# Optimization experiments

Measured on AMD Instinct MI355X. Metric: run time of the kernel, lower is better.

Reference implementation:

```python
import jax, jax.numpy as jnp
import numpy as np

B = 48            # graph pairs
NQ, NC = 20, 16   # query / corpus node counts (corpus padded to NMAX)
NMAX = 20         # max_node_set_size
DN, DE = 16, 8    # raw node / edge feature dims
D = 32            # node_state_dim
EH = 64           # edge_hidden_sizes[-1]
EQ, EC = 80, 60   # edges per query / corpus graph
PROP = 5          # n_prop_layers
TEMP = 0.01       # sinkhorn temperature
ITERS = 20        # sinkhorn iterations
LAMBDA = 1.0
NTOT = B * (NQ + NC)
NE = B * (EQ + EC)
SRC, DST = np.triu_indices(NMAX, 1)   # nC2 = 190 node pairs
_indq = np.ones(NMAX, np.int32)
_indc = np.array([1] * NC + [0] * (NMAX - NC), np.int32)
NXOR = jnp.asarray((_indq[:, None] ^ _indc[None, :]).astype(np.float32))  # [20,20]


def _mlp2(x, w1, b1, w2, b2):
    return jnp.maximum(x @ w1 + b1, 0.0) @ w2 + b2


def _sinkhorn(log_alpha):
    la = log_alpha / TEMP
    for _ in range(ITERS):
        la = la - jax.nn.logsumexp(la, axis=2, keepdims=True)
        la = la - jax.nn.logsumexp(la, axis=1, keepdims=True)
    return jnp.exp(la)


def _edge_emb(H, adj, w1, b1, w2, b2):
    s, d = H[:, SRC], H[:, DST]            # [B,nC2,D] gathers
    e = adj[:, SRC, DST][..., None]        # [B,nC2,1]
    f = _mlp2(jnp.concatenate([s, d, e], -1), w1, b1, w2, b2)
    bk = _mlp2(jnp.concatenate([d, s, e], -1), w1, b1, w2, b2)
    return f + bk                          # bidirectional msg, [B,nC2,EH]


def _forward(node_features, edge_features, query_adj, corpus_adj,
             enc_nw, enc_nb, enc_ew, enc_eb,
             msg_w1, msg_b1, msg_w2, msg_b2,
             upd_w1, upd_b1, upd_w2, upd_b2,
             sink_w1, sink_b1, sink_w2, sink_b2,
             lrl_w1, lrl_b1, lrl_w2, lrl_b2,
             from_idx, to_idx):
    h = node_features @ enc_nw + enc_nb    # GMN encoder (linear MLPs)
    e = edge_features @ enc_ew + enc_eb
    for _ in range(PROP):                  # shared-param propagation
        msg = _mlp2(jnp.concatenate([h[from_idx], h[to_idx], e], -1),
                    msg_w1, msg_b1, msg_w2, msg_b2)
        agg = jax.ops.segment_sum(msg, to_idx, num_segments=NTOT)
        h = h + _mlp2(jnp.concatenate([agg, h], -1), upd_w1, upd_b1, upd_w2, upd_b2)
    hp = h.reshape(B, NQ + NC, D)          # split_and_stack (static sizes)
    Hq = hp[:, :NQ]
    Hc = jnp.pad(hp[:, NQ:], ((0, 0), (0, NMAX - NC), (0, 0)))
    tq = _mlp2(Hq, sink_w1, sink_b1, sink_w2, sink_b2)
    tc = _mlp2(Hc, sink_w1, sink_b1, sink_w2, sink_b2)
    cost = jnp.abs(tq[:, :, None, :] - tc[:, None, :, :]).sum(-1)  # cdist p=1
    P = _sinkhorn(-cost)                   # node transport plan [B,20,20]
    Eq = _edge_emb(Hq, query_adj, lrl_w1, lrl_b1, lrl_w2, lrl_b2)
    Ec = _edge_emb(Hc, corpus_adj, lrl_w1, lrl_b1, lrl_w2, lrl_b2)
    Pa, Pb = P[:, SRC, :], P[:, DST, :]
    straight = Pa[:, :, SRC] * Pb[:, :, DST]    # plan[src_i,src_j]*plan[dst_i,dst_j]
    cross = Pa[:, :, DST] * Pb[:, :, SRC]
    eT = straight + cross                  # use_max=False, no second sinkhorn
    aq = query_adj[:, SRC, DST].astype(jnp.int32)
    ac = corpus_adj[:, SRC, DST].astype(jnp.int32)
    pxor = (aq[:, :, None] ^ ac[:, None, :]).astype(P.dtype)
    ediff = Eq[:, :, None, :] - Ec[:, None, :, :]   # [B,nC2,nC2,EH]
    ecost = jnp.maximum(ediff, 0.0).sum(-1) + jnp.maximum(-ediff, 0.0).sum(-1)
    edge_align = (pxor * eT * ecost).sum((-1, -2))
    ndiff = Hq[:, :, None, :] - Hc[:, None, :, :]   # [B,20,20,D]
    ncost = jnp.maximum(ndiff, 0.0).sum(-1) + jnp.maximum(-ndiff, 0.0).sum(-1)
    node_align = (NXOR * P * ncost).sum((-1, -2))
    return edge_align + LAMBDA * node_align         # [B]


def setup_inputs():
    key = jax.random.key(0)
    rng = np.random.default_rng(0)
    base = (np.arange(B) * (NQ + NC))[:, None]
    fq = base + rng.integers(0, NQ, (B, EQ)); tq = base + rng.integers(0, NQ, (B, EQ))
    fc = base + NQ + rng.integers(0, NC, (B, EC)); tc = base + NQ + rng.integers(0, NC, (B, EC))
    from_idx = jnp.asarray(np.concatenate([fq, fc], 1).reshape(-1), jnp.int32)
    to_idx = jnp.asarray(np.concatenate([tq, tc], 1).reshape(-1), jnp.int32)
    qadj = rng.integers(0, 2, (B, NMAX, NMAX)).astype(np.float32)
    cadj = rng.integers(0, 2, (B, NMAX, NMAX)).astype(np.float32)
    cadj[:, NC:, :] = 0.0; cadj[:, :, NC:] = 0.0   # padded corpus nodes have no edges
    ks = iter(jax.random.split(key, 32))
    def w(shape, s=0.1):
        return jax.random.normal(next(ks), shape, jnp.float32) * s
    return {
        'node_features': w((NTOT, DN), 1.0),
        'edge_features': w((NE, DE), 1.0),
        'query_adj': jnp.asarray(qadj),
        'corpus_adj': jnp.asarray(cadj),
        'enc_nw': w((DN, D)), 'enc_nb': w((D,)),
        'enc_ew': w((DE, 16)), 'enc_eb': w((16,)),
        'msg_w1': w((2 * D + 16, EH)), 'msg_b1': w((EH,)),
        'msg_w2': w((EH, EH)), 'msg_b2': w((EH,)),
        'upd_w1': w((EH + D, EH)), 'upd_b1': w((EH,)),
        'upd_w2': w((EH, D)), 'upd_b2': w((D,)),
        'sink_w1': w((D, NMAX)), 'sink_b1': w((NMAX,)),
        'sink_w2': w((NMAX, NMAX)), 'sink_b2': w((NMAX,)),
        'lrl_w1': w((2 * D + 1, EH)), 'lrl_b1': w((EH,)),
        'lrl_w2': w((EH, EH)), 'lrl_b2': w((EH,)),
        'from_idx': from_idx, 'to_idx': to_idx,
        'graph_sizes': jnp.asarray(np.tile([NQ, NC], B), jnp.int32),
    }


def reference(node_features, edge_features, query_adj, corpus_adj,
              enc_nw, enc_nb, enc_ew, enc_eb,
              msg_w1, msg_b1, msg_w2, msg_b2,
              upd_w1, upd_b1, upd_w2, upd_b2,
              sink_w1, sink_b1, sink_w2, sink_b2,
              lrl_w1, lrl_b1, lrl_w2, lrl_b2,
              from_idx, to_idx, graph_sizes):
    return _forward(node_features, edge_features, query_adj, corpus_adj,
                    enc_nw, enc_nb, enc_ew, enc_eb,
                    msg_w1, msg_b1, msg_w2, msg_b2,
                    upd_w1, upd_b1, upd_w2, upd_b2,
                    sink_w1, sink_b1, sink_w2, sink_b2,
                    lrl_w1, lrl_b1, lrl_w2, lrl_b2,
                    from_idx, to_idx)
```

## Files before the change

### kernel.cpp

```cpp
#include <hip/hip_runtime.h>


constexpr int kB    = 48;
constexpr int kNM   = 20;
constexpr int kD    = 32;
constexpr int kNP   = 190;
constexpr int kNTOT = 1728;
constexpr int kIters = 20;
constexpr float kInvT = 100.0f;

__device__ __forceinline__ void pair_sd(int p, int& s, int& d) {
    int row = 0, rem = p;
    #pragma unroll
    for (int r = 0; r < 19; ++r) {
        int len = 19 - r;
        if (rem < len) { row = r; break; }
        rem -= len;
    }
    s = row; d = row + 1 + rem;
}

__device__ __forceinline__ float bc(float v, int k) {
    return __int_as_float(__builtin_amdgcn_readlane(__float_as_int(v), k));
}

__device__ __forceinline__ void lse20(float (&r)[20]) {
    float m01 = fmaxf(r[0], r[1]),  m23 = fmaxf(r[2], r[3]),
          m45 = fmaxf(r[4], r[5]),  m67 = fmaxf(r[6], r[7]),
          m89 = fmaxf(r[8], r[9]),  mab = fmaxf(r[10], r[11]),
          mcd = fmaxf(r[12], r[13]), mef = fmaxf(r[14], r[15]),
          mgh = fmaxf(r[16], r[17]), mij = fmaxf(r[18], r[19]);
    float n0 = fmaxf(m01, m23), n1 = fmaxf(m45, m67), n2 = fmaxf(m89, mab),
          n3 = fmaxf(mcd, mef), n4 = fmaxf(mgh, mij);
    float m = fmaxf(fmaxf(fmaxf(n0, n1), fmaxf(n2, n3)), n4);
    float e[20];
    #pragma unroll
    for (int k = 0; k < 20; ++k) e[k] = __expf(r[k] - m);
    float s01 = e[0] + e[1],  s23 = e[2] + e[3],  s45 = e[4] + e[5],
          s67 = e[6] + e[7],  s89 = e[8] + e[9],  sab = e[10] + e[11],
          scd = e[12] + e[13], sef = e[14] + e[15], sgh = e[16] + e[17],
          sij = e[18] + e[19];
    float t0 = s01 + s23, t1 = s45 + s67, t2 = s89 + sab,
          t3 = scd + sef, t4 = sgh + sij;
    float s = ((t0 + t1) + (t2 + t3)) + t4;
    float l = m + __logf(s);
    #pragma unroll
    for (int k = 0; k < 20; ++k) r[k] -= l;
}

__global__ void k_enc(const float* __restrict__ nf, const float* __restrict__ nw,
                      const float* __restrict__ nb, const float* __restrict__ ef,
                      const float* __restrict__ ew, const float* __restrict__ eb,
                      float* __restrict__ h, float* __restrict__ ee,
                      float* __restrict__ agg, float* __restrict__ out) {
    int tid = blockIdx.x * 256 + threadIdx.x;
    int stride = gridDim.x * 256;
    for (int i = tid; i < kNTOT * 32; i += stride) {
        int n = i >> 5, c = i & 31;
        float acc = nb[c];
        const float* row = nf + n * 16;
        #pragma unroll
        for (int k = 0; k < 16; ++k) acc = fmaf(row[k], nw[k * 32 + c], acc);
        h[i] = acc;
    }
    for (int i = tid; i < 6720 * 16; i += stride) {
        int n = i >> 4, c = i & 15;
        float acc = eb[c];
        const float* row = ef + n * 8;
        #pragma unroll
        for (int k = 0; k < 8; ++k) acc = fmaf(row[k], ew[k * 16 + c], acc);
        ee[i] = acc;
    }
    for (int i = tid; i < kNTOT * 64; i += stride) agg[i] = 0.f;
    if (tid < kB) out[tid] = 0.f;
}

__global__ void __launch_bounds__(256)
k_msg(const float* __restrict__ h, const float* __restrict__ ee,
      const int* __restrict__ fidx, const int* __restrict__ tidx,
      const float* __restrict__ w1, const float* __restrict__ b1,
      const float* __restrict__ w2, const float* __restrict__ b2,
      float* __restrict__ agg) {
    int w = threadIdx.x >> 6, lane = threadIdx.x & 63;
    int e0 = (blockIdx.x * 4 + w) * 2;
    int toj[2]; float xa[2], xb[2], acc[2], o[2];
    #pragma unroll
    for (int j = 0; j < 2; ++j) {
        int e = e0 + j;
        int fr = fidx[e]; toj[j] = tidx[e];
        xa[j] = h[(lane < 32 ? fr : toj[j]) * kD + (lane & 31)];
        xb[j] = ee[e * 16 + (lane & 15)];
        acc[j] = b1[lane];
    }
    #pragma unroll
    for (int k = 0; k < 64; ++k) {
        float w1k = w1[k * 64 + lane];
        #pragma unroll
        for (int j = 0; j < 2; ++j) acc[j] = fmaf(bc(xa[j], k), w1k, acc[j]);
    }
    #pragma unroll
    for (int k = 0; k < 16; ++k) {
        float w1k = w1[(64 + k) * 64 + lane];
        #pragma unroll
        for (int j = 0; j < 2; ++j) acc[j] = fmaf(bc(xb[j], k), w1k, acc[j]);
    }
    #pragma unroll
    for (int j = 0; j < 2; ++j) { acc[j] = fmaxf(acc[j], 0.f); o[j] = b2[lane]; }
    #pragma unroll
    for (int k = 0; k < 64; ++k) {
        float w2k = w2[k * 64 + lane];
        #pragma unroll
        for (int j = 0; j < 2; ++j) o[j] = fmaf(bc(acc[j], k), w2k, o[j]);
    }
    #pragma unroll
    for (int j = 0; j < 2; ++j) atomicAdd(&agg[toj[j] * 64 + lane], o[j]);
}

__global__ void __launch_bounds__(256)
k_upd(float* __restrict__ h, float* __restrict__ agg,
      const float* __restrict__ w1, const float* __restrict__ b1,
      const float* __restrict__ w2, const float* __restrict__ b2) {
    int w = threadIdx.x >> 6, lane = threadIdx.x & 63;
    int n0 = (blockIdx.x * 4 + w) * 2;
    float xa[2], xb[2], acc[2], o[2];
    #pragma unroll
    for (int j = 0; j < 2; ++j) {
        int n = n0 + j;
        xa[j] = agg[n * 64 + lane];
        agg[n * 64 + lane] = 0.f;
        xb[j] = h[n * kD + (lane & 31)];
        acc[j] = b1[lane];
    }
    #pragma unroll
    for (int k = 0; k < 64; ++k) {
        float w1k = w1[k * 64 + lane];
        #pragma unroll
        for (int j = 0; j < 2; ++j) acc[j] = fmaf(bc(xa[j], k), w1k, acc[j]);
    }
    #pragma unroll
    for (int k = 0; k < 32; ++k) {
        float w1k = w1[(64 + k) * 64 + lane];
        #pragma unroll
        for (int j = 0; j < 2; ++j) acc[j] = fmaf(bc(xb[j], k), w1k, acc[j]);
    }
    #pragma unroll
    for (int j = 0; j < 2; ++j) { acc[j] = fmaxf(acc[j], 0.f); o[j] = b2[lane & 31]; }
    #pragma unroll
    for (int k = 0; k < 64; ++k) {
        float w2k = w2[k * 32 + (lane & 31)];
        #pragma unroll
        for (int j = 0; j < 2; ++j) o[j] = fmaf(bc(acc[j], k), w2k, o[j]);
    }
    if (lane < 32) {
        #pragma unroll
        for (int j = 0; j < 2; ++j) h[(n0 + j) * kD + lane] += o[j];
    }
}

__global__ void k_sink_t(const float* __restrict__ h,
                         const float* __restrict__ w1, const float* __restrict__ b1,
                         const float* __restrict__ w2, const float* __restrict__ b2,
                         float* __restrict__ Hq, float* __restrict__ Hc,
                         float* __restrict__ tq, float* __restrict__ tc) {
    __shared__ float xs[4][32];
    __shared__ float hs[4][20];
    int w = threadIdx.x >> 6, lane = threadIdx.x & 63;
    int xcd = blockIdx.x & 7, slot = blockIdx.x >> 3;
    int b = xcd + 8 * (slot / 10);
    int task = (slot % 10) * 4 + w;
    int side = task >= 20;
    int i = task - side * 20;
    if (lane < 32) {
        float v;
        if (side == 0) v = h[(b * 36 + i) * kD + lane];
        else           v = (i < 16) ? h[(b * 36 + 20 + i) * kD + lane] : 0.f;
        (side ? Hc : Hq)[(b * kNM + i) * kD + lane] = v;
        xs[w][lane] = v;
    }
    __syncthreads();
    if (lane < kNM) {
        float acc = b1[lane];
        #pragma unroll
        for (int k = 0; k < kD; ++k) acc += xs[w][k] * w1[k * kNM + lane];
        hs[w][lane] = fmaxf(acc, 0.f);
    }
    __syncthreads();
    if (lane < kNM) {
        float o = b2[lane];
        #pragma unroll
        for (int k = 0; k < kNM; ++k) o += hs[w][k] * w2[k * kNM + lane];
        (side ? tc : tq)[(b * kNM + i) * kNM + lane] = o;
    }
}

__global__ void k_sinkhorn(const float* __restrict__ tq, const float* __restrict__ tc,
                           const float* __restrict__ Hq,
                           float* __restrict__ P, float* __restrict__ out) {
    __shared__ float tcS[400];
    __shared__ float tr[20 * 21];
    int b = blockIdx.x, lane = threadIdx.x;
    for (int i = lane; i < 400; i += 64) tcS[i] = tc[b * 400 + i];
    int i20 = lane < 20 ? lane : 0;
    float tqr[20];
    #pragma unroll
    for (int k = 0; k < 20; ++k) tqr[k] = tq[(b * 20 + i20) * 20 + k];
    __syncthreads();
    float r[20];
    #pragma unroll
    for (int j = 0; j < 20; ++j) {
        float c = 0.f;
        #pragma unroll
        for (int k = 0; k < 20; ++k) c += fabsf(tqr[k] - tcS[j * 20 + k]);
        r[j] = -c * kInvT;
    }
    for (int it = 0; it < kIters; ++it) {
        lse20(r);
        if (lane < 20) {
            #pragma unroll
            for (int j = 0; j < 20; ++j) tr[lane * 21 + j] = r[j];
        }
        __syncthreads();
        if (lane < 20) {
            #pragma unroll
            for (int i = 0; i < 20; ++i) r[i] = tr[i * 21 + lane];
        }
        __syncthreads();
        lse20(r);
        if (lane < 20) {
            #pragma unroll
            for (int i = 0; i < 20; ++i) tr[i * 21 + lane] = r[i];
        }
        __syncthreads();
        if (lane < 20) {
            #pragma unroll
            for (int j = 0; j < 20; ++j) r[j] = tr[lane * 21 + j];
        }
        __syncthreads();
    }
    float part = 0.f;
    if (lane < 20) {
        float pv[20];
        #pragma unroll
        for (int j = 0; j < 20; ++j) pv[j] = __expf(r[j]);
        float* Pb = P + b * 400 + lane * 20;
        #pragma unroll
        for (int j = 0; j < 20; ++j) Pb[j] = pv[j];
        float pr4 = (pv[16] + pv[17]) + (pv[18] + pv[19]);
        float l1 = 0.f;
        const float* hq = Hq + (b * 20 + lane) * 32;
        #pragma unroll
        for (int k = 0; k < 32; ++k) l1 += fabsf(hq[k]);
        part = pr4 * l1;
    }
    #pragma unroll
    for (int off = 32; off; off >>= 1) part += __shfl_down(part, off, 64);
    if (lane == 0) atomicAdd(&out[b], part);
}

__global__ void __launch_bounds__(256)
k_edge_emb(const float* __restrict__ Hq, const float* __restrict__ Hc,
           const float* __restrict__ qadj, const float* __restrict__ cadj,
           const float* __restrict__ w1, const float* __restrict__ b1,
           const float* __restrict__ w2, const float* __restrict__ b2,
           float* __restrict__ Eq, float* __restrict__ Ec) {
    int w = threadIdx.x >> 6, lane = threadIdx.x & 63;
    int xcd = blockIdx.x & 7, slot = blockIdx.x >> 3;
    int b = xcd + 8 * (slot / 24);
    int r = slot % 24;
    float xa[4], ev[4], af[4], ab[4];
    int sidej[4], pj[4];
    #pragma unroll
    for (int j = 0; j < 4; ++j) {
        int tloc = r * 16 + w * 4 + j;
        if (tloc >= 380) tloc = 379;
        sidej[j] = tloc / kNP; pj[j] = tloc % kNP;
        int s, d; pair_sd(pj[j], s, d);
        const float* H = sidej[j] ? Hc : Hq;
        xa[j] = (lane < 32) ? H[(b * kNM + s) * kD + lane]
                            : H[(b * kNM + d) * kD + (lane - 32)];
        ev[j] = (sidej[j] ? cadj : qadj)[b * 400 + s * 20 + d];
        float bb = b1[lane];
        af[j] = bb; ab[j] = bb;
    }
    #pragma unroll
    for (int k = 0; k < 64; ++k) {
        float w1k = w1[k * 64 + lane];
        #pragma unroll
        for (int j = 0; j < 4; ++j) {
            af[j] = fmaf(bc(xa[j], k),      w1k, af[j]);
            ab[j] = fmaf(bc(xa[j], k ^ 32), w1k, ab[j]);
        }
    }
    {
        float w1e = w1[64 * 64 + lane];
        #pragma unroll
        for (int j = 0; j < 4; ++j) {
            af[j] = fmaf(ev[j], w1e, af[j]);
            ab[j] = fmaf(ev[j], w1e, ab[j]);
        }
    }
    float hid[4], o[4];
    #pragma unroll
    for (int j = 0; j < 4; ++j) {
        hid[j] = fmaxf(af[j], 0.f) + fmaxf(ab[j], 0.f);
        o[j] = 2.f * b2[lane];
    }
    #pragma unroll
    for (int k = 0; k < 64; ++k) {
        float w2k = w2[k * 64 + lane];
        #pragma unroll
        for (int j = 0; j < 4; ++j) o[j] = fmaf(bc(hid[j], k), w2k, o[j]);
    }
    #pragma unroll
    for (int j = 0; j < 4; ++j)
        (sidej[j] ? Ec : Eq)[(b * kNP + pj[j]) * 64 + lane] = o[j];
}

__global__ void __launch_bounds__(256, 4)
k_final(const float* __restrict__ P, const float* __restrict__ Eq,
        const float* __restrict__ Ec, const float* __restrict__ qadj,
        const float* __restrict__ cadj, float* __restrict__ out) {
    __shared__ float Ps[400];
    __shared__ unsigned char spsh[192], dpsh[192];
    int xcd = blockIdx.x & 7, slot = blockIdx.x >> 3;
    int b = xcd + 8 * (slot / 6), qt = slot % 6;
    int t = threadIdx.x, w = t >> 6, lane = t & 63;
    if (t < 192) {
        int s = 0, d = 0;
        if (t < kNP) pair_sd(t, s, d);
        spsh[t] = (unsigned char)s;
        dpsh[t] = (unsigned char)d;
    }
    for (int i = t; i < 400; i += 256) Ps[i] = P[b * 400 + i];
    __syncthreads();

    int l31 = lane & 31;
    int q = qt * 32 + l31;
    bool qv = q < kNP;
    int sq = spsh[qv ? q : 0], dq = dpsh[qv ? q : 0];
    float acv = qv ? cadj[b * 400 + sq * 20 + dq] : 0.f;

    float ec[32];
    #pragma unroll
    for (int j = 0; j < 32; ++j) {
        int qq = qt * 32 + j;
        ec[j] = (qq < kNP) ? Ec[(b * kNP + qq) * 64 + lane] : 0.f;
    }

    float a0 = 0.f, a1 = 0.f, a2 = 0.f, a3 = 0.f;
    int pp = w;
    float aqc = qadj[b * 400 + spsh[pp] * 20 + dpsh[pp]];
    float eqc = Eq[(b * kNP + pp) * 64 + lane];
    while (pp < kNP) {
        int pn = pp + 4;
        float aqn = 0.f, eqn = 0.f;
        if (pn < kNP) {
            aqn = qadj[b * 400 + spsh[pn] * 20 + dpsh[pn]];
            eqn = Eq[(b * kNP + pn) * 64 + lane];
        }
        int sp = spsh[pp], dp = dpsh[pp];
        float eT = Ps[sp * 20 + sq] * Ps[dp * 20 + dq]
                 + Ps[sp * 20 + dq] * Ps[dp * 20 + sq];
        float wqv = qv ? ((aqc > 0.5f) ? (1.f - acv) : acv) * eT : 0.f;
        #pragma unroll
        for (int j = 0; j < 32; j += 4) {
            a0 = fmaf(bc(wqv, j + 0), fabsf(eqc - ec[j + 0]), a0);
            a1 = fmaf(bc(wqv, j + 1), fabsf(eqc - ec[j + 1]), a1);
            a2 = fmaf(bc(wqv, j + 2), fabsf(eqc - ec[j + 2]), a2);
            a3 = fmaf(bc(wqv, j + 3), fabsf(eqc - ec[j + 3]), a3);
        }
        aqc = aqn; eqc = eqn; pp = pn;
    }
    float partial = (a0 + a1) + (a2 + a3);
    #pragma unroll
    for (int off = 32; off; off >>= 1) partial += __shfl_down(partial, off, 64);
    if (lane == 0) atomicAdd(&out[b], partial);
}

extern "C" void kernel_launch(void* const* d_in, const int* in_sizes, int n_in,
                              void* d_out, int out_size, void* d_ws, size_t ws_size,
                              hipStream_t stream) {
    auto f = [&](int i) { return (const float*)d_in[i]; };
    const float* nf   = f(0);
    const float* ef   = f(1);
    const float* qadj = f(2);
    const float* cadj = f(3);
    const int* from_idx = (const int*)d_in[24];
    const int* to_idx   = (const int*)d_in[25];
    float* out = (float*)d_out;

    float* ws  = (float*)d_ws;
    float* h   = ws;
    float* ee  = h   + 55296;
    float* agg = ee  + 107520;
    float* Hq  = agg + 110592;
    float* Hc  = Hq  + 30720;
    float* tq  = Hc  + 30720;
    float* tc  = tq  + 19200;
    float* P   = tc  + 19200;
    float* Eq  = P   + 19200;
    float* Ec  = Eq  + 583680;

    k_enc<<<432, 256, 0, stream>>>(nf, f(4), f(5), ef, f(6), f(7), h, ee, agg, out);
    for (int it = 0; it < 5; ++it) {
        k_msg<<<840, 256, 0, stream>>>(h, ee, from_idx, to_idx,
                                       f(8), f(9), f(10), f(11), agg);
        k_upd<<<216, 256, 0, stream>>>(h, agg, f(12), f(13), f(14), f(15));
    }
    k_sink_t<<<480, 256, 0, stream>>>(h, f(16), f(17), f(18), f(19), Hq, Hc, tq, tc);
    k_sinkhorn<<<48, 64, 0, stream>>>(tq, tc, Hq, P, out);
    k_edge_emb<<<1152, 256, 0, stream>>>(Hq, Hc, qadj, cadj,
                                         f(20), f(21), f(22), f(23), Eq, Ec);
    k_final<<<288, 256, 0, stream>>>(P, Eq, Ec, qadj, cadj, out);
}
```

Before: 152.1 us.

## Fuse message and update into per-node CSR gather kernel with ping-pong buffers

```diff
diff --git a/kernel.cpp b/kernel.cpp
--- a/kernel.cpp
+++ b/kernel.cpp
@@ -6,6 +6,7 @@
 constexpr int kD    = 32;
 constexpr int kNP   = 190;
 constexpr int kNTOT = 1728;
+constexpr int kNE   = 6720;
 constexpr int kIters = 20;
 constexpr float kInvT = 100.0f;
 
@@ -51,8 +52,8 @@
 __global__ void k_enc(const float* __restrict__ nf, const float* __restrict__ nw,
                       const float* __restrict__ nb, const float* __restrict__ ef,
                       const float* __restrict__ ew, const float* __restrict__ eb,
-                      float* __restrict__ h, float* __restrict__ ee,
-                      float* __restrict__ agg, float* __restrict__ out) {
+                      float* __restrict__ h0, float* __restrict__ ee,
+                      int* __restrict__ counts, float* __restrict__ out) {
     int tid = blockIdx.x * 256 + threadIdx.x;
     int stride = gridDim.x * 256;
     for (int i = tid; i < kNTOT * 32; i += stride) {
@@ -61,9 +62,9 @@
         const float* row = nf + n * 16;
         #pragma unroll
         for (int k = 0; k < 16; ++k) acc = fmaf(row[k], nw[k * 32 + c], acc);
-        h[i] = acc;
-    }
-    for (int i = tid; i < 6720 * 16; i += stride) {
+        h0[i] = acc;
+    }
+    for (int i = tid; i < kNE * 16; i += stride) {
         int n = i >> 4, c = i & 15;
         float acc = eb[c];
         const float* row = ef + n * 8;
@@ -71,90 +72,112 @@
         for (int k = 0; k < 8; ++k) acc = fmaf(row[k], ew[k * 16 + c], acc);
         ee[i] = acc;
     }
-    for (int i = tid; i < kNTOT * 64; i += stride) agg[i] = 0.f;
+    for (int i = tid; i < kNTOT; i += stride) counts[i] = 0;
     if (tid < kB) out[tid] = 0.f;
 }
 
+__global__ void k_count(const int* __restrict__ tidx, int* __restrict__ counts) {
+    int e = blockIdx.x * 256 + threadIdx.x;
+    if (e < kNE) atomicAdd(&counts[tidx[e]], 1);
+}
+
+__global__ void k_scan(const int* __restrict__ counts, int* __restrict__ offsets,
+                       int* __restrict__ cursor) {
+    int b = blockIdx.x, lane = threadIdx.x;
+    int c = (lane < 36) ? counts[b * 36 + lane] : 0;
+    int x = c;
+    #pragma unroll
+    for (int off = 1; off < 64; off <<= 1) {
+        int y = __shfl_up(x, off, 64);
+        if (lane >= off) x += y;
+    }
+    if (lane < 36) {
+        int o = b * 140 + x - c;
+        offsets[b * 36 + lane] = o;
+        cursor[b * 36 + lane]  = o;
+    }
+}
+
+__global__ void k_fill(const int* __restrict__ tidx, int* __restrict__ cursor,
+                       int* __restrict__ elist) {
+    int e = blockIdx.x * 256 + threadIdx.x;
+    if (e < kNE) {
+        int pos = atomicAdd(&cursor[tidx[e]], 1);
+        elist[pos] = e;
+    }
+}
+
 __global__ void __launch_bounds__(256)
-k_msg(const float* __restrict__ h, const float* __restrict__ ee,
-      const int* __restrict__ fidx, const int* __restrict__ tidx,
-      const float* __restrict__ w1, const float* __restrict__ b1,
-      const float* __restrict__ w2, const float* __restrict__ b2,
-      float* __restrict__ agg) {
-    int w = threadIdx.x >> 6, lane = threadIdx.x & 63;
-    int e0 = (blockIdx.x * 4 + w) * 2;
-    int toj[2]; float xa[2], xb[2], acc[2], o[2];
-    #pragma unroll
-    for (int j = 0; j < 2; ++j) {
-        int e = e0 + j;
-        int fr = fidx[e]; toj[j] = tidx[e];
-        xa[j] = h[(lane < 32 ? fr : toj[j]) * kD + (lane & 31)];
-        xb[j] = ee[e * 16 + (lane & 15)];
-        acc[j] = b1[lane];
-    }
-    #pragma unroll
-    for (int k = 0; k < 64; ++k) {
-        float w1k = w1[k * 64 + lane];
-        #pragma unroll
-        for (int j = 0; j < 2; ++j) acc[j] = fmaf(bc(xa[j], k), w1k, acc[j]);
-    }
-    #pragma unroll
-    for (int k = 0; k < 16; ++k) {
-        float w1k = w1[(64 + k) * 64 + lane];
-        #pragma unroll
-        for (int j = 0; j < 2; ++j) acc[j] = fmaf(bc(xb[j], k), w1k, acc[j]);
-    }
-    #pragma unroll
-    for (int j = 0; j < 2; ++j) { acc[j] = fmaxf(acc[j], 0.f); o[j] = b2[lane]; }
-    #pragma unroll
-    for (int k = 0; k < 64; ++k) {
-        float w2k = w2[k * 64 + lane];
-        #pragma unroll
-        for (int j = 0; j < 2; ++j) o[j] = fmaf(bc(acc[j], k), w2k, o[j]);
-    }
-    #pragma unroll
-    for (int j = 0; j < 2; ++j) atomicAdd(&agg[toj[j] * 64 + lane], o[j]);
-}
-
-__global__ void __launch_bounds__(256)
-k_upd(float* __restrict__ h, float* __restrict__ agg,
-      const float* __restrict__ w1, const float* __restrict__ b1,
-      const float* __restrict__ w2, const float* __restrict__ b2) {
-    int w = threadIdx.x >> 6, lane = threadIdx.x & 63;
-    int n0 = (blockIdx.x * 4 + w) * 2;
-    float xa[2], xb[2], acc[2], o[2];
-    #pragma unroll
-    for (int j = 0; j < 2; ++j) {
-        int n = n0 + j;
-        xa[j] = agg[n * 64 + lane];
-        agg[n * 64 + lane] = 0.f;
-        xb[j] = h[n * kD + (lane & 31)];
-        acc[j] = b1[lane];
-    }
-    #pragma unroll
-    for (int k = 0; k < 64; ++k) {
-        float w1k = w1[k * 64 + lane];
-        #pragma unroll
-        for (int j = 0; j < 2; ++j) acc[j] = fmaf(bc(xa[j], k), w1k, acc[j]);
-    }
-    #pragma unroll
-    for (int k = 0; k < 32; ++k) {
-        float w1k = w1[(64 + k) * 64 + lane];
-        #pragma unroll
-        for (int j = 0; j < 2; ++j) acc[j] = fmaf(bc(xb[j], k), w1k, acc[j]);
-    }
-    #pragma unroll
-    for (int j = 0; j < 2; ++j) { acc[j] = fmaxf(acc[j], 0.f); o[j] = b2[lane & 31]; }
-    #pragma unroll
-    for (int k = 0; k < 64; ++k) {
-        float w2k = w2[k * 32 + (lane & 31)];
-        #pragma unroll
-        for (int j = 0; j < 2; ++j) o[j] = fmaf(bc(acc[j], k), w2k, o[j]);
-    }
-    if (lane < 32) {
-        #pragma unroll
-        for (int j = 0; j < 2; ++j) h[(n0 + j) * kD + lane] += o[j];
-    }
+k_msgupd(const float* __restrict__ hc, float* __restrict__ hn_out,
+         const float* __restrict__ ee,
+         const int* __restrict__ fidx, const int* __restrict__ elist,
+         const int* __restrict__ offsets, const int* __restrict__ counts,
+         const float* __restrict__ mw1, const float* __restrict__ mb1,
+         const float* __restrict__ mw2, const float* __restrict__ mb2,
+         const float* __restrict__ uw1, const float* __restrict__ ub1,
+         const float* __restrict__ uw2, const float* __restrict__ ub2) {
+    int lane = threadIdx.x & 63;
+    int n = blockIdx.x * 4 + (threadIdx.x >> 6);
+    int deg = counts[n], base = offsets[n];
+    float hn = hc[n * 32 + (lane & 31)];
+    float msum = 0.f;
+    int i = 0;
+    for (; i + 1 < deg; i += 2) {
+        int e0 = elist[base + i], e1 = elist[base + i + 1];
+        int f0 = fidx[e0], f1 = fidx[e1];
+        float xa0 = (lane < 32) ? hc[f0 * 32 + lane] : hn;
+        float xa1 = (lane < 32) ? hc[f1 * 32 + lane] : hn;
+        float xb0 = ee[e0 * 16 + (lane & 15)];
+        float xb1 = ee[e1 * 16 + (lane & 15)];
+        float a0 = mb1[lane], a1 = a0;
+        #pragma unroll
+        for (int k = 0; k < 64; ++k) {
+            float w = mw1[k * 64 + lane];
+            a0 = fmaf(bc(xa0, k), w, a0);
+            a1 = fmaf(bc(xa1, k), w, a1);
+        }
+        #pragma unroll
+        for (int k = 0; k < 16; ++k) {
+            float w = mw1[(64 + k) * 64 + lane];
+            a0 = fmaf(bc(xb0, k), w, a0);
+            a1 = fmaf(bc(xb1, k), w, a1);
+        }
+        a0 = fmaxf(a0, 0.f); a1 = fmaxf(a1, 0.f);
+        float o0 = mb2[lane], o1 = o0;
+        #pragma unroll
+        for (int k = 0; k < 64; ++k) {
+            float w = mw2[k * 64 + lane];
+            o0 = fmaf(bc(a0, k), w, o0);
+            o1 = fmaf(bc(a1, k), w, o1);
+        }
+        msum += o0 + o1;
+    }
+    if (i < deg) {
+        int e0 = elist[base + i];
+        int f0 = fidx[e0];
+        float xa0 = (lane < 32) ? hc[f0 * 32 + lane] : hn;
+        float xb0 = ee[e0 * 16 + (lane & 15)];
+        float a0 = mb1[lane];
+        #pragma unroll
+        for (int k = 0; k < 64; ++k) a0 = fmaf(bc(xa0, k), mw1[k * 64 + lane], a0);
+        #pragma unroll
+        for (int k = 0; k < 16; ++k) a0 = fmaf(bc(xb0, k), mw1[(64 + k) * 64 + lane], a0);
+        a0 = fmaxf(a0, 0.f);
+        float o0 = mb2[lane];
+        #pragma unroll
+        for (int k = 0; k < 64; ++k) o0 = fmaf(bc(a0, k), mw2[k * 64 + lane], o0);
+        msum += o0;
+    }
+    float acc = ub1[lane];
+    #pragma unroll
+    for (int k = 0; k < 64; ++k) acc = fmaf(bc(msum, k), uw1[k * 64 + lane], acc);
+    #pragma unroll
+    for (int k = 0; k < 32; ++k) acc = fmaf(bc(hn, k), uw1[(64 + k) * 64 + lane], acc);
+    acc = fmaxf(acc, 0.f);
+    float o = ub2[lane & 31];
+    #pragma unroll
+    for (int k = 0; k < 64; ++k) o = fmaf(bc(acc, k), uw2[k * 32 + (lane & 31)], o);
+    if (lane < 32) hn_out[n * 32 + lane] = hn + o;
 }
 
 __global__ void k_sink_t(const float* __restrict__ h,
@@ -316,6 +339,10 @@
         (sidej[j] ? Ec : Eq)[(b * kNP + pj[j]) * 64 + lane] = o[j];
 }
 
+#define EC_ALL(X) X(0) X(1) X(2) X(3) X(4) X(5) X(6) X(7) X(8) X(9) X(10) X(11) \
+  X(12) X(13) X(14) X(15) X(16) X(17) X(18) X(19) X(20) X(21) X(22) X(23) \
+  X(24) X(25) X(26) X(27) X(28) X(29) X(30) X(31)
+
 __global__ void __launch_bounds__(256, 4)
 k_final(const float* __restrict__ P, const float* __restrict__ Eq,
         const float* __restrict__ Ec, const float* __restrict__ qadj,
@@ -340,12 +367,10 @@
     int sq = spsh[qv ? q : 0], dq = dpsh[qv ? q : 0];
     float acv = qv ? cadj[b * 400 + sq * 20 + dq] : 0.f;
 
-    float ec[32];
-    #pragma unroll
-    for (int j = 0; j < 32; ++j) {
-        int qq = qt * 32 + j;
-        ec[j] = (qq < kNP) ? Ec[(b * kNP + qq) * 64 + lane] : 0.f;
-    }
+    const float* ecb = Ec + (b * kNP + qt * 32) * 64 + lane;
+#define EC_DECL(i) float ec##i = (qt * 32 + i < kNP) ? ecb[i * 64] : 0.f;
+    EC_ALL(EC_DECL)
+#undef EC_DECL
 
     float a0 = 0.f, a1 = 0.f, a2 = 0.f, a3 = 0.f;
     int pp = w;
@@ -362,13 +387,13 @@
         float eT = Ps[sp * 20 + sq] * Ps[dp * 20 + dq]
                  + Ps[sp * 20 + dq] * Ps[dp * 20 + sq];
         float wqv = qv ? ((aqc > 0.5f) ? (1.f - acv) : acv) * eT : 0.f;
-        #pragma unroll
-        for (int j = 0; j < 32; j += 4) {
-            a0 = fmaf(bc(wqv, j + 0), fabsf(eqc - ec[j + 0]), a0);
-            a1 = fmaf(bc(wqv, j + 1), fabsf(eqc - ec[j + 1]), a1);
-            a2 = fmaf(bc(wqv, j + 2), fabsf(eqc - ec[j + 2]), a2);
-            a3 = fmaf(bc(wqv, j + 3), fabsf(eqc - ec[j + 3]), a3);
-        }
+#define EC_FMA(i) { float d_ = fabsf(eqc - ec##i); \
+        if ((i & 3) == 0) a0 = fmaf(bc(wqv, i), d_, a0); \
+        else if ((i & 3) == 1) a1 = fmaf(bc(wqv, i), d_, a1); \
+        else if ((i & 3) == 2) a2 = fmaf(bc(wqv, i), d_, a2); \
+        else a3 = fmaf(bc(wqv, i), d_, a3); }
+        EC_ALL(EC_FMA)
+#undef EC_FMA
         aqc = aqn; eqc = eqn; pp = pn;
     }
     float partial = (a0 + a1) + (a2 + a3);
@@ -390,24 +415,34 @@
     float* out = (float*)d_out;
 
     float* ws  = (float*)d_ws;
-    float* h   = ws;
-    float* ee  = h   + 55296;
-    float* agg = ee  + 107520;
-    float* Hq  = agg + 110592;
-    float* Hc  = Hq  + 30720;
-    float* tq  = Hc  + 30720;
-    float* tc  = tq  + 19200;
-    float* P   = tc  + 19200;
-    float* Eq  = P   + 19200;
-    float* Ec  = Eq  + 583680;
-
-    k_enc<<<432, 256, 0, stream>>>(nf, f(4), f(5), ef, f(6), f(7), h, ee, agg, out);
+    float* h0  = ws;
+    float* h1  = h0 + 55296;
+    float* ee  = h1 + 55296;
+    float* Hq  = ee + 107520;
+    float* Hc  = Hq + 30720;
+    float* tq  = Hc + 30720;
+    float* tc  = tq + 19200;
+    float* P   = tc + 19200;
+    float* Eq  = P  + 19200;
+    float* Ec  = Eq + 583680;
+    int* counts  = (int*)(Ec + 583680);
+    int* offsets = counts + kNTOT;
+    int* cursor  = offsets + kNTOT;
+    int* elist   = cursor + kNTOT;
+
+    k_enc<<<432, 256, 0, stream>>>(nf, f(4), f(5), ef, f(6), f(7), h0, ee, counts, out);
+    k_count<<<27, 256, 0, stream>>>(to_idx, counts);
+    k_scan<<<48, 64, 0, stream>>>(counts, offsets, cursor);
+    k_fill<<<27, 256, 0, stream>>>(to_idx, cursor, elist);
+    float* hc = h0;
+    float* hn = h1;
     for (int it = 0; it < 5; ++it) {
-        k_msg<<<840, 256, 0, stream>>>(h, ee, from_idx, to_idx,
-                                       f(8), f(9), f(10), f(11), agg);
-        k_upd<<<216, 256, 0, stream>>>(h, agg, f(12), f(13), f(14), f(15));
-    }
-    k_sink_t<<<480, 256, 0, stream>>>(h, f(16), f(17), f(18), f(19), Hq, Hc, tq, tc);
+        k_msgupd<<<432, 256, 0, stream>>>(hc, hn, ee, from_idx, elist, offsets, counts,
+                                          f(8), f(9), f(10), f(11),
+                                          f(12), f(13), f(14), f(15));
+        float* tmp = hc; hc = hn; hn = tmp;
+    }
+    k_sink_t<<<480, 256, 0, stream>>>(hc, f(16), f(17), f(18), f(19), Hq, Hc, tq, tc);
     k_sinkhorn<<<48, 64, 0, stream>>>(tq, tc, Hq, P, out);
     k_edge_emb<<<1152, 256, 0, stream>>>(Hq, Hc, qadj, cadj,
                                          f(20), f(21), f(22), f(23), Eq, Ec);
```

Measured after the change: 187.5 us. +23.3%, slower.
